# Optimization experiments

Hardware: AMD Instinct MI355X
Metric: run time of the kernel (lower is better)

Reference implementation:

```python
import jax, jax.numpy as jnp
import numpy as np

B, C, T, L, H = 1024, 32, 9, 24, 8
D = C // H
TOKEN_LEN = 24

def _l2norm(x, eps=1e-12):
    n = jnp.linalg.norm(x, axis=-1, keepdims=True)
    return x / jnp.maximum(n, eps)

def setup_inputs() -> dict:
    key = jax.random.key(0)
    ks = jax.random.split(key, 16)
    def lin_w(k, din, dout):
        return (jax.random.uniform(k, (din, dout), jnp.float32) - 0.5) * (2.0 / np.sqrt(din))
    def lin_b(k, dout, din):
        return (jax.random.uniform(k, (dout,), jnp.float32) - 0.5) * (2.0 / np.sqrt(din))
    inp = {}
    inp['x'] = jax.random.normal(ks[0], (B, C, T, L), jnp.float32)
    inp['Wq'] = lin_w(ks[1], C, C); inp['bq'] = lin_b(ks[2], C, C)
    inp['Wk'] = lin_w(ks[3], C, C); inp['bk'] = lin_b(ks[4], C, C)
    inp['Wv'] = lin_w(ks[5], C, C); inp['bv'] = lin_b(ks[6], C, C)
    inp['Wm'] = lin_w(ks[7], C, C); inp['bm'] = lin_b(ks[8], C, C)
    inp['W_logit'] = jnp.eye(H, dtype=jnp.float32)
    inp['W_ctx'] = jnp.eye(H, dtype=jnp.float32)
    inp['rel_pos_bias'] = jax.random.normal(ks[9], (H, 2 * TOKEN_LEN - 1), jnp.float32) * 0.02
    inp['pre_prompt'] = jax.random.normal(ks[10], (1, C, T, TOKEN_LEN), jnp.float32) * 0.02
    inp['conv_w'] = jax.random.normal(ks[11], (C, C, 3, 3), jnp.float32) / np.sqrt(C * 9)
    inp['conv_b'] = jnp.zeros((C,), jnp.float32)
    inp['bn_gamma'] = jnp.ones((C,), jnp.float32)
    inp['bn_beta'] = jnp.zeros((C,), jnp.float32)
    inp['bn_mean'] = jax.random.normal(ks[12], (C,), jnp.float32) * 0.1
    inp['bn_var'] = jax.random.uniform(ks[13], (C,), jnp.float32) * 0.5 + 0.75
    inp['p_w'] = lin_w(ks[14], TOKEN_LEN, 6).T  # torch Linear(24,6) weight: (6,24)
    inp['p_b'] = lin_b(ks[15], 6, TOKEN_LEN)
    inp['atten_flag'] = 2
    return inp

def reference(x, Wq, bq, Wk, bk, Wv, bv, Wm, bm, W_logit, W_ctx, rel_pos_bias,
              pre_prompt, conv_w, conv_b, bn_gamma, bn_beta, bn_mean, bn_var,
              p_w, p_b, atten_flag):
    b, c, t, l = x.shape
    xp = jnp.transpose(x, (0, 2, 3, 1))  # (b,t,l,c)
    def heads(W, bias):
        y = xp @ W + bias
        return jnp.transpose(y.reshape(b, t, l, H, D), (0, 1, 3, 2, 4))  # (b,t,h,l,d)
    q = _l2norm(heads(Wq, bq))
    k = _l2norm(heads(Wk, bk))
    v = _l2norm(heads(Wv, bv))
    logits = jnp.einsum('bthid,bthjd->bthij', q, k) / np.sqrt(D).astype(np.float32)
    idx = jnp.arange(l)
    rel = jnp.clip(idx[:, None] - idx[None, :] + TOKEN_LEN - 1, 0, 2 * TOKEN_LEN - 2)
    logits = logits + rel_pos_bias[:, rel][None, None]  # bias: (h,l,l)
    logits = jnp.einsum('bthij,hH->btHij', logits, W_logit)
    attn = jax.nn.softmax(logits, axis=-1)
    attn = jnp.einsum('bthij,hH->btHij', attn, W_ctx)
    x_att = jnp.einsum('bthij,bthjd->bthid', attn, v)
    x_att = jnp.transpose(x_att, (0, 1, 3, 2, 4)).reshape(b, t, l, c) @ Wm + bm
    x_att = jnp.transpose(x_att, (0, 3, 1, 2))  # (b,c,t,l)
    pre = jnp.broadcast_to(pre_prompt, (b, c, t, l))
    if atten_flag == 1:
        con = jnp.concatenate([x_att[..., :18], pre[..., 18:]], -1); tar = x_att[..., 18:]
    elif atten_flag == 2:
        con = jnp.concatenate([x_att[..., :12], pre[..., 12:18], x_att[..., 18:]], -1); tar = x_att[..., 12:18]
    elif atten_flag == 3:
        con = jnp.concatenate([x_att[..., :6], pre[..., 6:12], x_att[..., 12:]], -1); tar = x_att[..., 6:12]
    else:
        con = jnp.concatenate([pre[..., :6], x_att[..., 6:]], -1); tar = x_att[..., :6]
    # ConvNormAct(32,32,3,1): Conv2d(3x3, same pad) + BatchNorm2d(eval) + ReLU
    y = jax.lax.conv_general_dilated(con, conv_w, (1, 1), 'SAME',
                                     dimension_numbers=('NCHW', 'OIHW', 'NCHW'))
    y = y + conv_b[None, :, None, None]
    y = (y - bn_mean[None, :, None, None]) * jax.lax.rsqrt(bn_var[None, :, None, None] + 1e-5)
    y = y * bn_gamma[None, :, None, None] + bn_beta[None, :, None, None]
    y = jax.nn.relu(y)
    p = jnp.einsum('bctl,ol->bcto', y, p_w) + p_b  # Linear(token_len, 6) on last dim
    p = tar - p
    if atten_flag == 1:
        out = jnp.concatenate([x_att[..., :18], p], -1)
    elif atten_flag == 2:
        out = jnp.concatenate([x_att[..., :12], p, x_att[..., 18:]], -1)
    elif atten_flag == 3:
        out = jnp.concatenate([x_att[..., :6], p, x_att[..., 12:]], -1)
    else:
        out = jnp.concatenate([p, x_att[..., 6:]], -1)
    return out  # dropout is identity in eval mode
```

## Files before the change

kernel.cpp:

```cpp
#include <hip/hip_runtime.h>
#include <hip/hip_bf16.h>

#define NB   1024
#define NC   32
#define NT   9
#define NL   24
#define CTL  6912
#define TOK  216
#define QSTR 880
#define VROW 220
#define NTHR 1024

typedef _Float16 f16x8 __attribute__((ext_vector_type(8)));
typedef _Float16 f16x4 __attribute__((ext_vector_type(4)));
typedef _Float16 f16x2 __attribute__((ext_vector_type(2)));
typedef float    f32x4 __attribute__((ext_vector_type(4)));

#define OFF_BIGA 0
#define SZ_BIGA  42240
#define OFF_XATT (OFF_BIGA + 28160)
#define OFF_BIGB (OFF_BIGA + SZ_BIGA)
#define OFF_WM   (OFF_BIGB + 7680)
#define OFF_BIGC (OFF_WM + 2560)
#define OFF_SPRE (OFF_BIGC + 20480)
#define OFF_REL  (OFF_SPRE + 4320)
#define OFF_WL   (OFF_REL + 1504)
#define OFF_WC   (OFF_WL + 256)
#define OFF_BQKV (OFF_WC + 256)
#define OFF_BM   (OFF_BQKV + 384)
#define OFF_AC   (OFF_BM + 128)
#define OFF_BC   (OFF_AC + 128)
#define OFF_PW   (OFF_BC + 128)
#define OFF_PB   (OFF_PW + 576)
#define OFF_FLG  (OFF_PB + 24)
#define POOL_SZ  80672

static __device__ __forceinline__ float ldf(const void* p, size_t i, bool f32) {
    return f32 ? ((const float*)p)[i]
               : __bfloat162float(((const __hip_bfloat16*)p)[i]);
}
static __device__ __forceinline__ void stf(void* p, size_t i, float v, bool f32) {
    if (f32) ((float*)p)[i] = v;
    else     ((__hip_bfloat16*)p)[i] = __float2bfloat16(v);
}
static __device__ __forceinline__ f32x4 mfma16(f16x8 a, f16x8 b, f32x4 c) {
    return __builtin_amdgcn_mfma_f32_16x16x32_f16(a, b, c, 0, 0, 0);
}
static __device__ __forceinline__ float fdot2(f16x2 a, f16x2 b, float c) {
#if __has_builtin(__builtin_amdgcn_fdot2)
    return __builtin_amdgcn_fdot2(a, b, c, false);
#else
    return c + (float)a[0]*(float)b[0] + (float)a[1]*(float)b[1];
#endif
}
static __device__ __forceinline__ f16x2 pack2(float lo, float hi) {
#if __has_builtin(__builtin_amdgcn_cvt_pkrtz)
    return __builtin_bit_cast(f16x2, __builtin_amdgcn_cvt_pkrtz(lo, hi));
#else
    f16x2 r; r[0] = (_Float16)lo; r[1] = (_Float16)hi; return r;
#endif
}
static __device__ __forceinline__ float rsq_f(float x) {
#if __has_builtin(__builtin_amdgcn_rsqf)
    return __builtin_amdgcn_rsqf(x);
#else
    return rsqrtf(x);
#endif
}
static __device__ __forceinline__ float rcp_f(float x) {
#if __has_builtin(__builtin_amdgcn_rcpf)
    return __builtin_amdgcn_rcpf(x);
#else
    return 1.0f / x;
#endif
}

__global__ __launch_bounds__(NTHR, 8) void fused_kernel(
    const void* __restrict__ x,
    const void* __restrict__ Wq, const void* __restrict__ bq,
    const void* __restrict__ Wk, const void* __restrict__ bk,
    const void* __restrict__ Wv, const void* __restrict__ bv,
    const void* __restrict__ Wm, const void* __restrict__ bm,
    const void* __restrict__ Wl, const void* __restrict__ Wc,
    const void* __restrict__ rel, const void* __restrict__ pre,
    const void* __restrict__ cw, const void* __restrict__ cb,
    const void* __restrict__ gmm, const void* __restrict__ bta,
    const void* __restrict__ mean, const void* __restrict__ var,
    const void* __restrict__ p_w, const void* __restrict__ p_b,
    const int* __restrict__ atten_flag,
    void* __restrict__ out)
{
    __shared__ __align__(16) char pool[POOL_SZ];

    const bool f32p = (((const unsigned*)Wl)[0] == 0x3F800000u);
    const int tid  = threadIdx.x;
    const int b    = blockIdx.x;
    const int lane = tid & 63;
    const int wave = tid >> 6;
    const int l15  = lane & 15;
    const int quad = lane >> 4;
    const int grp  = lane & ~7;

    const int flag = atten_flag[0];
    const int s = (flag == 1) ? 18 : (flag == 2) ? 12 : (flag == 3) ? 6 : 0;

    {
        _Float16* xT  = (_Float16*)(pool + OFF_BIGA);
        _Float16* atH = (_Float16*)(pool + OFF_BIGC);
        _Float16* Wqk = (_Float16*)(pool + OFF_BIGB);
        _Float16* WmH = (_Float16*)(pool + OFF_WM);
        _Float16* prH = (_Float16*)(pool + OFF_SPRE);
        float* relF = (float*)(pool + OFF_REL);
        float* wlF  = (float*)(pool + OFF_WL);
        float* wcF  = (float*)(pool + OFF_WC);
        float* bqk  = (float*)(pool + OFF_BQKV);
        float* bmF  = (float*)(pool + OFF_BM);
        float* acF  = (float*)(pool + OFF_AC);
        float* bcF  = (float*)(pool + OFF_BC);
        float* pwF  = (float*)(pool + OFF_PW);
        float* pbF  = (float*)(pool + OFF_PB);

        if (f32p) {
            const float* xb = (const float*)x + (size_t)b*CTL;
            for (int idx = tid; idx < 1728; idx += NTHR) {
                int tok = idx >> 3, g = idx & 7;
                f16x4 v;
                #pragma unroll
                for (int k = 0; k < 4; k++)
                    v[k] = (_Float16)xb[(g*4 + k)*TOK + tok];
                *(f16x4*)(xT + tok*40 + g*4) = v;
            }
            for (int i4 = tid; i4 < 768; i4 += NTHR) {
                int mat = i4 >> 8, r4 = i4 & 255;
                int ci = r4 >> 3, co = (r4 & 7) << 2;
                const void* W = (mat == 0) ? Wq : (mat == 1) ? Wk : Wv;
                float4 v = ((const float4*)W)[r4];
                _Float16* dst = Wqk + (mat*32 + co)*40 + ci;
                dst[0]   = (_Float16)v.x;
                dst[40]  = (_Float16)v.y;
                dst[80]  = (_Float16)v.z;
                dst[120] = (_Float16)v.w;
            }
            for (int i4 = tid; i4 < 256; i4 += NTHR) {
                int ci = i4 >> 3, co = (i4 & 7) << 2;
                float4 v = ((const float4*)Wm)[i4];
                _Float16* dst = WmH + co*40 + ci;
                dst[0]   = (_Float16)v.x;
                dst[40]  = (_Float16)v.y;
                dst[80]  = (_Float16)v.z;
                dst[120] = (_Float16)v.w;
            }
        } else {
            for (int i = tid; i < CTL; i += NTHR) {
                int c = i / TOK, tok = i % TOK;
                xT[tok*40 + c] = (_Float16)ldf(x, (size_t)b*CTL + i, f32p);
            }
            for (int i = tid; i < 3072; i += NTHR) {
                int mat = i >> 10, r = i & 1023, ci = r >> 5, co = r & 31;
                const void* W = (mat == 0) ? Wq : (mat == 1) ? Wk : Wv;
                Wqk[(mat*32 + co)*40 + ci] = (_Float16)ldf(W, r, f32p);
            }
            for (int i = tid; i < 1024; i += NTHR) {
                int ci = i >> 5, co = i & 31;
                WmH[co*40 + ci] = (_Float16)ldf(Wm, i, f32p);
            }
        }
        for (int i = tid; i < 1600; i += NTHR) {
            xT[8640 + i]  = (_Float16)0.f;
            atH[8640 + i] = (_Float16)0.f;
        }
        for (int idx = tid; idx < 432; idx += NTHR) {
            int row = idx >> 3, g = idx & 7;
            int tt = row / 6, o = row % 6;
            f16x4 v;
            #pragma unroll
            for (int k = 0; k < 4; k++) {
                int ci = g*4 + k;
                v[k] = (_Float16)ldf(pre, (ci*9 + tt)*24 + s + o, f32p);
            }
            *(f16x4*)(prH + row*40 + g*4) = v;
        }
        for (int i = tid; i < 376; i += NTHR) relF[i] = ldf(rel, i, f32p);
        if (tid < 64)  wlF[tid] = ldf(Wl, tid, f32p);
        if (tid >= 64 && tid < 128) wcF[tid-64] = ldf(Wc, tid-64, f32p);
        if (tid >= 128 && tid < 224) {
            int i = tid - 128; int mat = i >> 5;
            const void* bb = (mat == 0) ? bq : (mat == 1) ? bk : bv;
            bqk[i] = ldf(bb, i & 31, f32p);
        }
        if (tid >= 224 && tid < 256) bmF[tid-224] = ldf(bm, tid-224, f32p);
        if (tid < 32) {
            float rs = rsqrtf(ldf(var, tid, f32p) + 1e-5f);
            float A  = ldf(gmm, tid, f32p) * rs;
            acF[tid] = A;
            bcF[tid] = (ldf(cb, tid, f32p) - ldf(mean, tid, f32p)) * A
                       + ldf(bta, tid, f32p);
        }
        if (tid >= 32 && tid < 176) pwF[tid-32] = ldf(p_w, tid-32, f32p);
        if (tid >= 176 && tid < 182) pbF[tid-176] = ldf(p_b, tid-176, f32p);
    }
    __syncthreads();

    if (tid < 2) {
        const float* M = (const float*)(pool + (tid == 0 ? OFF_WL : OFF_WC));
        int id = 1;
        for (int i = 0; i < 64; i++)
            id &= (M[i] == ((i % 9 == 0) ? 1.f : 0.f));
        ((int*)(pool + OFF_FLG))[tid] = id;
    }

    {
        const _Float16* xT  = (const _Float16*)(pool + OFF_BIGA);
        const _Float16* Wqk = (const _Float16*)(pool + OFF_BIGB);
        f32x4 acc[6];
        #pragma unroll
        for (int nt = 0; nt < 6; nt++) acc[nt] = 0.f;
        f16x8 bfr[6];
        #pragma unroll
        for (int nt = 0; nt < 6; nt++)
            bfr[nt] = *(const f16x8*)(Wqk + (nt*16 + l15)*40 + quad*8);
        const int mt = wave;
        if (mt < 14) {
            f16x8 a = *(const f16x8*)(xT + (mt*16 + l15)*40 + quad*8);
            #pragma unroll
            for (int nt = 0; nt < 6; nt++)
                acc[nt] = mfma16(a, bfr[nt], acc[nt]);
        }
        __syncthreads();
        _Float16* qH = (_Float16*)(pool + OFF_BIGA);
        const float* bqk = (const float*)(pool + OFF_BQKV);
        if (mt < 14) {
            #pragma unroll
            for (int nt = 0; nt < 6; nt++) {
                int co = nt*16 + l15;
                int mat = co >> 5, hc = co & 31;
                float bias = bqk[co];
                if (mat < 2) {
                    _Float16* dst = qH + (mat*8 + (hc >> 2))*QSTR + (hc & 3);
                    #pragma unroll
                    for (int r = 0; r < 4; r++) {
                        int tok = mt*16 + quad*4 + r;
                        if (tok < 216) dst[tok*4] = (_Float16)(acc[nt][r] + bias);
                    }
                } else {
                    _Float16* dst = qH + (16 + (hc >> 2))*QSTR + (hc & 3)*VROW;
                    #pragma unroll
                    for (int r = 0; r < 4; r++) {
                        int tok = mt*16 + quad*4 + r;
                        if (tok < 216) dst[tok] = (_Float16)(acc[nt][r] + bias);
                    }
                }
            }
        }
    }
    __syncthreads();

    {
        _Float16* qH = (_Float16*)(pool + OFF_BIGA);
        for (int idx = tid; idx < 16*216; idx += NTHR) {
            int plane = idx / 216, tok = idx % 216;
            f16x4* pv = (f16x4*)(qH + plane*QSTR + tok*4);
            f16x4 v = *pv;
            float a0 = v[0], a1 = v[1], a2 = v[2], a3 = v[3];
            float s2 = a0*a0 + a1*a1 + a2*a2 + a3*a3;
            float sc = ((plane < 8) ? 0.5f : 1.0f) * rsq_f(fmaxf(s2, 1e-24f));
            f16x4 nv;
            nv[0] = (_Float16)(a0*sc); nv[1] = (_Float16)(a1*sc);
            nv[2] = (_Float16)(a2*sc); nv[3] = (_Float16)(a3*sc);
            *pv = nv;
        }
        for (int idx = tid; idx < 8*216; idx += NTHR) {
            int h = idx / 216, tok = idx % 216;
            _Float16* vp = qH + (16 + h)*QSTR + tok;
            float a0 = vp[0], a1 = vp[VROW], a2 = vp[2*VROW], a3 = vp[3*VROW];
            float s2 = a0*a0 + a1*a1 + a2*a2 + a3*a3;
            float sc = rsq_f(fmaxf(s2, 1e-24f));
            vp[0]      = (_Float16)(a0*sc);
            vp[VROW]   = (_Float16)(a1*sc);
            vp[2*VROW] = (_Float16)(a2*sc);
            vp[3*VROW] = (_Float16)(a3*sc);
        }
    }
    __syncthreads();

    {
        const int idWl = ((int*)(pool + OFF_FLG))[0];
        const int idWc = ((int*)(pool + OFF_FLG))[1];
        const _Float16* qH = (const _Float16*)(pool + OFF_BIGA);
        _Float16* attH = (_Float16*)(pool + OFF_BIGC);
        const float* srel = (const float*)(pool + OFF_REL);
        const float* wlF  = (const float*)(pool + OFF_WL);
        const float* wcF  = (const float*)(pool + OFF_WC);

        for (int idx = tid; idx < 1728; idx += NTHR) {
            int t = idx / 192, r = idx % 192, i = r >> 3, h = r & 7;
            int tb = t * 24;
            const f16x2* qp = (const f16x2*)(qH + h*QSTR + (tb + i)*4);
            f16x2 q01 = qp[0], q23 = qp[1];
            const _Float16* kB = qH + (8 + h)*QSTR + tb*4;
            const float* rl = srel + h*47 + i + 23;
            float sc[24];
            #pragma unroll
            for (int j = 0; j < 24; j++) {
                const f16x2* kp = (const f16x2*)(kB + j*4);
                sc[j] = fdot2(q01, kp[0], fdot2(q23, kp[1], rl[-j]));
            }
            if (!idWl) {
                float wl[8], mx[24];
                #pragma unroll
                for (int hh = 0; hh < 8; hh++) wl[hh] = wlF[hh*8 + h];
                #pragma unroll
                for (int j = 0; j < 24; j++) mx[j] = 0.f;
                #pragma unroll
                for (int hh = 0; hh < 8; hh++) {
                    float c = wl[hh];
                    #pragma unroll
                    for (int j = 0; j < 24; j++)
                        mx[j] += c * __shfl(sc[j], grp + hh);
                }
                #pragma unroll
                for (int j = 0; j < 24; j++) sc[j] = mx[j];
            }
            float ssum = 0.f;
            #pragma unroll
            for (int j = 0; j < 24; j++) { sc[j] = __expf(sc[j]); ssum += sc[j]; }
            float inv = rcp_f(ssum);
            #pragma unroll
            for (int j = 0; j < 24; j++) sc[j] *= inv;
            if (!idWc) {
                float wc8[8], mx[24];
                #pragma unroll
                for (int hh = 0; hh < 8; hh++) wc8[hh] = wcF[hh*8 + h];
                #pragma unroll
                for (int j = 0; j < 24; j++) mx[j] = 0.f;
                #pragma unroll
                for (int hh = 0; hh < 8; hh++) {
                    float c = wc8[hh];
                    #pragma unroll
                    for (int j = 0; j < 24; j++)
                        mx[j] += c * __shfl(sc[j], grp + hh);
                }
                #pragma unroll
                for (int j = 0; j < 24; j++) sc[j] = mx[j];
            }
            f16x2 pa[12];
            #pragma unroll
            for (int jp = 0; jp < 12; jp++)
                pa[jp] = pack2(sc[2*jp], sc[2*jp + 1]);
            const _Float16* vbase = qH + (16 + h)*QSTR + tb;
            float o[4];
            #pragma unroll
            for (int d = 0; d < 4; d++) {
                const f16x4* vr = (const f16x4*)(vbase + d*VROW);
                float od = 0.f;
                #pragma unroll
                for (int jj = 0; jj < 6; jj++) {
                    f16x4 vv = vr[jj];
                    f16x2 vlo = __builtin_shufflevector(vv, vv, 0, 1);
                    f16x2 vhi = __builtin_shufflevector(vv, vv, 2, 3);
                    od = fdot2(pa[2*jj],     vlo, od);
                    od = fdot2(pa[2*jj + 1], vhi, od);
                }
                o[d] = od;
            }
            f16x4 ov;
            ov[0] = (_Float16)o[0]; ov[1] = (_Float16)o[1];
            ov[2] = (_Float16)o[2]; ov[3] = (_Float16)o[3];
            *(f16x4*)(attH + (tb + i)*40 + h*4) = ov;
        }
    }
    __syncthreads();

    f32x4 acc4[2];
    {
        const _Float16* aH  = (const _Float16*)(pool + OFF_BIGC);
        const _Float16* WmH = (const _Float16*)(pool + OFF_WM);
        acc4[0] = 0.f; acc4[1] = 0.f;
        f16x8 bf2[2];
        #pragma unroll
        for (int nt = 0; nt < 2; nt++)
            bf2[nt] = *(const f16x8*)(WmH + (nt*16 + l15)*40 + quad*8);
        const int mt = wave;
        if (mt < 14) {
            f16x8 a = *(const f16x8*)(aH + (mt*16 + l15)*40 + quad*8);
            acc4[0] = mfma16(a, bf2[0], acc4[0]);
            acc4[1] = mfma16(a, bf2[1], acc4[1]);
        }
        _Float16* cwH = (_Float16*)(pool + OFF_BIGA);
        if (f32p) {
            const float* cwf = (const float*)cw;
            for (int idx = tid; idx < 2304; idx += NTHR) {
                int row = idx >> 3, g = idx & 7;
                int sh = row >> 5, co = row & 31;
                f16x4 v;
                #pragma unroll
                for (int k = 0; k < 4; k++)
                    v[k] = (_Float16)cwf[co*288 + (g*4 + k)*9 + sh];
                *(f16x4*)(cwH + row*40 + g*4) = v;
            }
        } else {
            for (int i = tid; i < 9216; i += NTHR) {
                int co = i / 288, rr = i % 288, ci = rr / 9, sh = rr % 9;
                cwH[(sh*32 + co)*40 + ci] = (_Float16)ldf(cw, i, f32p);
            }
        }
    }
    __syncthreads();
    {
        _Float16* sconH = (_Float16*)(pool + OFF_BIGC);
        _Float16* xattT = (_Float16*)(pool + OFF_XATT);
        float* starF = (float*)(pool + OFF_BIGB);
        const float* bmF = (const float*)(pool + OFF_BM);
        const int mt = wave;
        if (mt < 14) {
            #pragma unroll
            for (int nt = 0; nt < 2; nt++) {
                int co = nt*16 + l15;
                float bias = bmF[co];
                #pragma unroll
                for (int r = 0; r < 4; r++) {
                    int tok = mt*16 + quad*4 + r;
                    if (tok < 216) {
                        float v = acc4[nt][r] + bias;
                        _Float16 vh = (_Float16)v;
                        sconH[tok*40 + co] = vh;
                        xattT[co*VROW + tok] = vh;
                        int t = tok / 24, l = tok % 24, lo = l - s;
                        if (lo >= 0 && lo < 6) starF[(co*9 + t)*6 + lo] = v;
                    }
                }
            }
        }
    }
    __syncthreads();

    f32x4 accc[2];
    {
        const _Float16* sconH = (const _Float16*)(pool + OFF_BIGC);
        const _Float16* prH   = (const _Float16*)(pool + OFF_SPRE);
        const _Float16* cwH   = (const _Float16*)(pool + OFF_BIGA);
        accc[0] = 0.f; accc[1] = 0.f;
        const int mt = wave;
        int tok0 = mt*16 + l15;
        int ok = tok0 < 216;
        int tc = ok ? tok0 : 0;
        int tA = tc / 24, lA = tc % 24;
        f16x8 zf = 0;
        for (int sh = 0; sh < 9; sh++) {
            int dt = sh/3 - 1, dl = sh%3 - 1;
            f16x8 b0 = *(const f16x8*)(cwH + (sh*32 + l15)*40 + quad*8);
            f16x8 b1 = *(const f16x8*)(cwH + (sh*32 + 16 + l15)*40 + quad*8);
            if (mt < 14) {
                int tt = tA + dt, ll = lA + dl;
                bool valid = ok && tt >= 0 && tt < 9 && ll >= 0 && ll < 24;
                int ttc = valid ? tt : 0, llc = valid ? ll : 0;
                bool inT = (llc >= s) && (llc < s + 6);
                const _Float16* ab = inT ? (prH + (ttc*6 + (llc - s))*40)
                                         : (sconH + (ttc*24 + llc)*40);
                f16x8 a = *(const f16x8*)(ab + quad*8);
                if (!valid) a = zf;
                accc[0] = mfma16(a, b0, accc[0]);
                accc[1] = mfma16(a, b1, accc[1]);
            }
        }
    }
    __syncthreads();
    {
        float* yF = (float*)(pool + OFF_BIGA);
        const float* acF = (const float*)(pool + OFF_AC);
        const float* bcF = (const float*)(pool + OFF_BC);
        const int mt = wave;
        if (mt < 14) {
            #pragma unroll
            for (int nt = 0; nt < 2; nt++) {
                int co = nt*16 + l15;
                float A = acF[co], Bc = bcF[co];
                #pragma unroll
                for (int r = 0; r < 4; r++) {
                    int tok = mt*16 + quad*4 + r;
                    if (tok < 216) {
                        int t = tok / 24, l = tok % 24;
                        yF[(co*9 + t)*24 + l] = fmaxf(accc[nt][r]*A + Bc, 0.f);
                    }
                }
            }
        }
    }
    __syncthreads();

    {
        const float* yF  = (const float*)(pool + OFF_BIGA);
        float* starF     = (float*)(pool + OFF_BIGB);
        const float* pwF = (const float*)(pool + OFF_PW);
        const float* pbF = (const float*)(pool + OFF_PB);
        for (int idx = tid; idx < NC*NT*6; idx += NTHR) {
            int co = idx / 54, r = idx % 54, t = r / 6, o = r % 6;
            const f32x4* yr = (const f32x4*)(yF + (co*9 + t)*24);
            const f32x4* pw = (const f32x4*)(pwF + o*24);
            f32x4 s4 = yr[0] * pw[0];
            #pragma unroll
            for (int l4 = 1; l4 < 6; l4++) s4 += yr[l4] * pw[l4];
            float p = pbF[o] + s4[0] + s4[1] + s4[2] + s4[3];
            starF[idx] = starF[idx] - p;
        }
    }
    __syncthreads();

    {
        const _Float16* xattT = (const _Float16*)(pool + OFF_XATT);
        const float* resF = (const float*)(pool + OFF_BIGB);
        if (f32p) {
            float* of = (float*)out + (size_t)b*CTL;
            for (int i4 = tid; i4 < CTL/4; i4 += NTHR) {
                int i = i4 * 4;
                int co = i / TOK, tok0 = i % TOK;
                f16x4 xa = *(const f16x4*)(xattT + co*VROW + tok0);
                int t = tok0 / 24, l0 = tok0 % 24;
                float4 v;
                float* vp = (float*)&v;
                #pragma unroll
                for (int k = 0; k < 4; k++) {
                    int lo = l0 + k - s;
                    vp[k] = (lo >= 0 && lo < 6) ? resF[(co*9 + t)*6 + lo]
                                                : (float)xa[k];
                }
                *(float4*)(of + i) = v;
            }
        } else {
            for (int i = tid; i < CTL; i += NTHR) {
                int co = i / TOK, tok = i % TOK;
                int t = tok / 24, l = tok % 24, lo = l - s;
                float v = (lo >= 0 && lo < 6) ? resF[(co*9 + t)*6 + lo]
                                              : (float)xattT[co*VROW + tok];
                stf(out, (size_t)b*CTL + i, v, f32p);
            }
        }
    }
}

extern "C" void kernel_launch(void* const* d_in, const int* in_sizes, int n_in,
                              void* d_out, int out_size, void* d_ws, size_t ws_size,
                              hipStream_t stream) {
    (void)d_ws; (void)ws_size; (void)in_sizes; (void)n_in; (void)out_size;
    fused_kernel<<<NB, NTHR, 0, stream>>>(
        d_in[0], d_in[1], d_in[2], d_in[3], d_in[4], d_in[5], d_in[6],
        d_in[7], d_in[8], d_in[9], d_in[10], d_in[11], d_in[12], d_in[13],
        d_in[14], d_in[15], d_in[16], d_in[17], d_in[18], d_in[19], d_in[20],
        (const int*)d_in[21], d_out);
}
```

Measured before the change: 181.0 us.

## Load x directly into MFMA registers and fuse L2 norm into projection epilogue

The x tile is now loaded from global memory straight into the MFMA A-operand registers, so the LDS transpose staging of x and one barrier are gone. L2 normalisation of q, k and v is folded into the projection epilogue using lane shuffles, which removes a separate LDS pass and another barrier. Softmax now uses exp2, with the log2(e) factor folded into the q scale and the relative-position bias. In exchange, the global loads of x are strided per lane rather than coalesced, and the normalisation arithmetic is repeated across lanes.

```diff
diff --git a/kernel.cpp b/kernel.cpp
--- a/kernel.cpp
+++ b/kernel.cpp
@@ -74,6 +74,13 @@
     return 1.0f / x;
 #endif
 }
+static __device__ __forceinline__ float ex2(float x) {
+#if __has_builtin(__builtin_amdgcn_exp2f)
+    return __builtin_amdgcn_exp2f(x);
+#else
+    return exp2f(x);
+#endif
+}
 
 __global__ __launch_bounds__(NTHR, 8) void fused_kernel(
     const void* __restrict__ x,
@@ -103,9 +110,22 @@
 
     const int flag = atten_flag[0];
     const int s = (flag == 1) ? 18 : (flag == 2) ? 12 : (flag == 3) ? 6 : 0;
-
-    {
-        _Float16* xT  = (_Float16*)(pool + OFF_BIGA);
+    const float L2E = 1.4426950408889634f;
+
+    f16x8 aReg;
+    {
+        int tok = wave*16 + l15;
+        bool okk = tok < 216;
+        int tokc = okk ? tok : 215;
+        size_t base = (size_t)b*CTL + tokc;
+        #pragma unroll
+        for (int k = 0; k < 8; k++) {
+            float v = ldf(x, base + (size_t)(quad*8 + k)*TOK, f32p);
+            aReg[k] = okk ? (_Float16)v : (_Float16)0.f;
+        }
+    }
+
+    {
         _Float16* atH = (_Float16*)(pool + OFF_BIGC);
         _Float16* Wqk = (_Float16*)(pool + OFF_BIGB);
         _Float16* WmH = (_Float16*)(pool + OFF_WM);
@@ -121,15 +141,6 @@
         float* pbF  = (float*)(pool + OFF_PB);
 
         if (f32p) {
-            const float* xb = (const float*)x + (size_t)b*CTL;
-            for (int idx = tid; idx < 1728; idx += NTHR) {
-                int tok = idx >> 3, g = idx & 7;
-                f16x4 v;
-                #pragma unroll
-                for (int k = 0; k < 4; k++)
-                    v[k] = (_Float16)xb[(g*4 + k)*TOK + tok];
-                *(f16x4*)(xT + tok*40 + g*4) = v;
-            }
             for (int i4 = tid; i4 < 768; i4 += NTHR) {
                 int mat = i4 >> 8, r4 = i4 & 255;
                 int ci = r4 >> 3, co = (r4 & 7) << 2;
@@ -151,10 +162,6 @@
                 dst[120] = (_Float16)v.w;
             }
         } else {
-            for (int i = tid; i < CTL; i += NTHR) {
-                int c = i / TOK, tok = i % TOK;
-                xT[tok*40 + c] = (_Float16)ldf(x, (size_t)b*CTL + i, f32p);
-            }
             for (int i = tid; i < 3072; i += NTHR) {
                 int mat = i >> 10, r = i & 1023, ci = r >> 5, co = r & 31;
                 const void* W = (mat == 0) ? Wq : (mat == 1) ? Wk : Wv;
@@ -165,10 +172,8 @@
                 WmH[co*40 + ci] = (_Float16)ldf(Wm, i, f32p);
             }
         }
-        for (int i = tid; i < 1600; i += NTHR) {
-            xT[8640 + i]  = (_Float16)0.f;
+        for (int i = tid; i < 1600; i += NTHR)
             atH[8640 + i] = (_Float16)0.f;
-        }
         for (int idx = tid; idx < 432; idx += NTHR) {
             int row = idx >> 3, g = idx & 7;
             int tt = row / 6, o = row % 6;
@@ -180,7 +185,7 @@
             }
             *(f16x4*)(prH + row*40 + g*4) = v;
         }
-        for (int i = tid; i < 376; i += NTHR) relF[i] = ldf(rel, i, f32p);
+        for (int i = tid; i < 376; i += NTHR) relF[i] = ldf(rel, i, f32p) * L2E;
         if (tid < 64)  wlF[tid] = ldf(Wl, tid, f32p);
         if (tid >= 64 && tid < 128) wcF[tid-64] = ldf(Wc, tid-64, f32p);
         if (tid >= 128 && tid < 224) {
@@ -210,7 +215,6 @@
     }
 
     {
-        const _Float16* xT  = (const _Float16*)(pool + OFF_BIGA);
         const _Float16* Wqk = (const _Float16*)(pool + OFF_BIGB);
         f32x4 acc[6];
         #pragma unroll
@@ -219,66 +223,37 @@
         #pragma unroll
         for (int nt = 0; nt < 6; nt++)
             bfr[nt] = *(const f16x8*)(Wqk + (nt*16 + l15)*40 + quad*8);
-        const int mt = wave;
-        if (mt < 14) {
-            f16x8 a = *(const f16x8*)(xT + (mt*16 + l15)*40 + quad*8);
+        if (wave < 14) {
             #pragma unroll
             for (int nt = 0; nt < 6; nt++)
-                acc[nt] = mfma16(a, bfr[nt], acc[nt]);
-        }
-        __syncthreads();
+                acc[nt] = mfma16(aReg, bfr[nt], acc[nt]);
+        }
         _Float16* qH = (_Float16*)(pool + OFF_BIGA);
         const float* bqk = (const float*)(pool + OFF_BQKV);
-        if (mt < 14) {
+        if (wave < 14) {
             #pragma unroll
             for (int nt = 0; nt < 6; nt++) {
                 int co = nt*16 + l15;
                 int mat = co >> 5, hc = co & 31;
                 float bias = bqk[co];
-                if (mat < 2) {
-                    _Float16* dst = qH + (mat*8 + (hc >> 2))*QSTR + (hc & 3);
-                    #pragma unroll
-                    for (int r = 0; r < 4; r++) {
-                        int tok = mt*16 + quad*4 + r;
-                        if (tok < 216) dst[tok*4] = (_Float16)(acc[nt][r] + bias);
+                float scl0 = (mat == 0) ? 0.5f * L2E : 1.0f;
+                #pragma unroll
+                for (int r = 0; r < 4; r++) {
+                    int tok = wave*16 + quad*4 + r;
+                    float v = acc[nt][r] + bias;
+                    float sq = v*v;
+                    sq += __shfl_xor(sq, 1);
+                    sq += __shfl_xor(sq, 2);
+                    float scn = scl0 * rsq_f(fmaxf(sq, 1e-24f));
+                    _Float16 vh = (_Float16)(v * scn);
+                    if (tok < 216) {
+                        if (mat < 2)
+                            qH[(mat*8 + (hc >> 2))*QSTR + (hc & 3) + tok*4] = vh;
+                        else
+                            qH[(16 + (hc >> 2))*QSTR + (hc & 3)*VROW + tok] = vh;
                     }
-                } else {
-                    _Float16* dst = qH + (16 + (hc >> 2))*QSTR + (hc & 3)*VROW;
-                    #pragma unroll
-                    for (int r = 0; r < 4; r++) {
-                        int tok = mt*16 + quad*4 + r;
-                        if (tok < 216) dst[tok] = (_Float16)(acc[nt][r] + bias);
-                    }
-                }
-            }
-        }
-    }
-    __syncthreads();
-
-    {
-        _Float16* qH = (_Float16*)(pool + OFF_BIGA);
-        for (int idx = tid; idx < 16*216; idx += NTHR) {
-            int plane = idx / 216, tok = idx % 216;
-            f16x4* pv = (f16x4*)(qH + plane*QSTR + tok*4);
-            f16x4 v = *pv;
-            float a0 = v[0], a1 = v[1], a2 = v[2], a3 = v[3];
-            float s2 = a0*a0 + a1*a1 + a2*a2 + a3*a3;
-            float sc = ((plane < 8) ? 0.5f : 1.0f) * rsq_f(fmaxf(s2, 1e-24f));
-            f16x4 nv;
-            nv[0] = (_Float16)(a0*sc); nv[1] = (_Float16)(a1*sc);
-            nv[2] = (_Float16)(a2*sc); nv[3] = (_Float16)(a3*sc);
-            *pv = nv;
-        }
-        for (int idx = tid; idx < 8*216; idx += NTHR) {
-            int h = idx / 216, tok = idx % 216;
-            _Float16* vp = qH + (16 + h)*QSTR + tok;
-            float a0 = vp[0], a1 = vp[VROW], a2 = vp[2*VROW], a3 = vp[3*VROW];
-            float s2 = a0*a0 + a1*a1 + a2*a2 + a3*a3;
-            float sc = rsq_f(fmaxf(s2, 1e-24f));
-            vp[0]      = (_Float16)(a0*sc);
-            vp[VROW]   = (_Float16)(a1*sc);
-            vp[2*VROW] = (_Float16)(a2*sc);
-            vp[3*VROW] = (_Float16)(a3*sc);
+                }
+            }
         }
     }
     __syncthreads();
@@ -323,7 +298,7 @@
             }
             float ssum = 0.f;
             #pragma unroll
-            for (int j = 0; j < 24; j++) { sc[j] = __expf(sc[j]); ssum += sc[j]; }
+            for (int j = 0; j < 24; j++) { sc[j] = ex2(sc[j]); ssum += sc[j]; }
             float inv = rcp_f(ssum);
             #pragma unroll
             for (int j = 0; j < 24; j++) sc[j] *= inv;
@@ -380,9 +355,8 @@
         #pragma unroll
         for (int nt = 0; nt < 2; nt++)
             bf2[nt] = *(const f16x8*)(WmH + (nt*16 + l15)*40 + quad*8);
-        const int mt = wave;
-        if (mt < 14) {
-            f16x8 a = *(const f16x8*)(aH + (mt*16 + l15)*40 + quad*8);
+        if (wave < 14) {
+            f16x8 a = *(const f16x8*)(aH + (wave*16 + l15)*40 + quad*8);
             acc4[0] = mfma16(a, bf2[0], acc4[0]);
             acc4[1] = mfma16(a, bf2[1], acc4[1]);
         }
@@ -411,15 +385,14 @@
         _Float16* xattT = (_Float16*)(pool + OFF_XATT);
         float* starF = (float*)(pool + OFF_BIGB);
         const float* bmF = (const float*)(pool + OFF_BM);
-        const int mt = wave;
-        if (mt < 14) {
+        if (wave < 14) {
             #pragma unroll
             for (int nt = 0; nt < 2; nt++) {
                 int co = nt*16 + l15;
                 float bias = bmF[co];
                 #pragma unroll
                 for (int r = 0; r < 4; r++) {
-                    int tok = mt*16 + quad*4 + r;
+                    int tok = wave*16 + quad*4 + r;
                     if (tok < 216) {
                         float v = acc4[nt][r] + bias;
                         _Float16 vh = (_Float16)v;
@@ -440,8 +413,7 @@
         const _Float16* prH   = (const _Float16*)(pool + OFF_SPRE);
         const _Float16* cwH   = (const _Float16*)(pool + OFF_BIGA);
         accc[0] = 0.f; accc[1] = 0.f;
-        const int mt = wave;
-        int tok0 = mt*16 + l15;
+        int tok0 = wave*16 + l15;
         int ok = tok0 < 216;
         int tc = ok ? tok0 : 0;
         int tA = tc / 24, lA = tc % 24;
@@ -450,7 +422,7 @@
             int dt = sh/3 - 1, dl = sh%3 - 1;
             f16x8 b0 = *(const f16x8*)(cwH + (sh*32 + l15)*40 + quad*8);
             f16x8 b1 = *(const f16x8*)(cwH + (sh*32 + 16 + l15)*40 + quad*8);
-            if (mt < 14) {
+            if (wave < 14) {
                 int tt = tA + dt, ll = lA + dl;
                 bool valid = ok && tt >= 0 && tt < 9 && ll >= 0 && ll < 24;
                 int ttc = valid ? tt : 0, llc = valid ? ll : 0;
@@ -469,15 +441,14 @@
         float* yF = (float*)(pool + OFF_BIGA);
         const float* acF = (const float*)(pool + OFF_AC);
         const float* bcF = (const float*)(pool + OFF_BC);
-        const int mt = wave;
-        if (mt < 14) {
+        if (wave < 14) {
             #pragma unroll
             for (int nt = 0; nt < 2; nt++) {
                 int co = nt*16 + l15;
                 float A = acF[co], Bc = bcF[co];
                 #pragma unroll
                 for (int r = 0; r < 4; r++) {
-                    int tok = mt*16 + quad*4 + r;
+                    int tok = wave*16 + quad*4 + r;
                     if (tok < 216) {
                         int t = tok / 24, l = tok % 24;
                         yF[(co*9 + t)*24 + l] = fmaxf(accc[nt][r]*A + Bc, 0.f);
```

Result: faster. 174.8 us (-3.4%).
